# Kernel optimization log

Measured on AMD Instinct MI355X. Metric: run time of the kernel, lower is better.

## Reference

```python
import jax, jax.numpy as jnp
import numpy as np

B, C, H, W = 2, 48, 64, 64
EPS = 1e-5
ROW = [0, 0, 0, H // 4, H // 4, H // 4, H // 2, H // 2, H // 2]
COL = [0, W // 4, W // 2] * 3


def setup_inputs() -> dict:
    key = jax.random.key(0)
    ks = iter(jax.random.split(key, 40))
    s = 1.0 / np.sqrt(C)  # keep unscaled-softmax logits sane
    def rn(shape, scale=1.0):
        return jax.random.normal(next(ks), shape, jnp.float32) * scale
    def ru(shape):
        return jax.random.uniform(next(ks), shape, jnp.float32, 0.5, 1.5)
    return dict(
        input_feature=rn((B, C, H, W)), feat_b=rn((B, C, H, W)),
        feat_c=rn((B, C, H, W)), feat_d=rn((B, C, H, W)),
        W_fa_all=rn((C, C), s), W_fb_all=rn((C, C), s),
        W_fc_all=rn((C, C), s), W_fd_all=rn((C, C), s),
        W_fa=rn((9, C, C), s), W_fb=rn((9, C, C), s),
        W_fc=rn((9, C, C), s), W_fd=rn((9, C, C), s),
        fuse_w=rn((C, 4 * C), s), fuse_b=rn((C,), 0.1),
        fuse_g=ru((C,)), fuse_bb=rn((C,), 0.1), fuse_m=rn((C,), 0.1), fuse_v=ru((C,)),
        fuseP_w=rn((9, C, 4 * C), s), fuseP_b=rn((9, C), 0.1),
        fuseP_g=ru((9, C)), fuseP_bb=rn((9, C), 0.1), fuseP_m=rn((9, C), 0.1), fuseP_v=ru((9, C)),
        gamma_all=rn(()), gamma_p=rn((9,)),
        out_w=rn((C, C, 3, 3), s / 3.0), out_b=rn((C,), 0.1),
        out_g=ru((C,)), out_bb=rn((C,), 0.1), out_m=rn((C,), 0.1), out_v=ru((C,)),
    )


def _attn(q, k, v):
    # q,k,v: [..., C, N] -> energy [..., N, N]; non-standard softmax(max - energy)
    e = jnp.einsum('...cn,...cm->...nm', q, k)
    e = jnp.max(e, axis=-1, keepdims=True) - e
    a = jax.nn.softmax(e, axis=-1)
    return jnp.einsum('...cn,...nm->...cm', v, a)  # torch.matmul(v, attention)


def reference(input_feature, feat_b, feat_c, feat_d,
              W_fa_all, W_fb_all, W_fc_all, W_fd_all,
              W_fa, W_fb, W_fc, W_fd,
              fuse_w, fuse_b, fuse_g, fuse_bb, fuse_m, fuse_v,
              fuseP_w, fuseP_b, fuseP_g, fuseP_bb, fuseP_m, fuseP_v,
              gamma_all, gamma_p,
              out_w, out_b, out_g, out_bb, out_m, out_v):
    h2, w2 = H // 2, W // 2
    N = H * W
    # ---- global branch: channel-wise Linear (bias=False) applied over spatial tokens
    fa = jnp.einsum('dc,bcn->bdn', W_fa_all, input_feature.reshape(B, C, N))
    fb = jnp.einsum('dc,bcn->bdn', W_fb_all, feat_b.reshape(B, C, N))
    fc = jnp.einsum('dc,bcn->bdn', W_fc_all, feat_c.reshape(B, C, N))
    fd = jnp.einsum('dc,bcn->bdn', W_fd_all, feat_d.reshape(B, C, N))
    cat = jnp.concatenate([_attn(fa, fa, fa), _attn(fa, fb, fb),
                           _attn(fa, fc, fc), _attn(fa, fd, fd)], axis=1)
    cat = cat.reshape(B, 4 * C, H, W)
    y = jnp.einsum('oc,bchw->bohw', fuse_w, cat) + fuse_b[None, :, None, None]
    y = (y - fuse_m[:, None, None]) * (fuse_g / jnp.sqrt(fuse_v + EPS))[:, None, None] + fuse_bb[:, None, None]
    atten_all = jax.nn.relu(y)  # Dropout2d is identity at eval
    # ---- 9 overlapping patch branches, vectorized over the patch axis p
    def crops(x):
        return jnp.stack([x[:, :, r:r + h2, c:c + w2] for r, c in zip(ROW, COL)], 0).reshape(9, B, C, h2 * w2)
    pa = jnp.einsum('pdc,pbcn->pbdn', W_fa, crops(input_feature))
    pb = jnp.einsum('pdc,pbcn->pbdn', W_fb, crops(feat_b))
    pc = jnp.einsum('pdc,pbcn->pbdn', W_fc, crops(feat_c))
    pd = jnp.einsum('pdc,pbcn->pbdn', W_fd, crops(feat_d))
    pcat = jnp.concatenate([_attn(pa, pa, pa), _attn(pa, pb, pb),
                            _attn(pa, pc, pc), _attn(pa, pd, pd)], axis=2)
    pcat = pcat.reshape(9, B, 4 * C, h2, w2)
    py = jnp.einsum('poc,pbchw->pbohw', fuseP_w, pcat) + fuseP_b[:, None, :, None, None]
    py = ((py - fuseP_m[:, None, :, None, None])
          * (fuseP_g / jnp.sqrt(fuseP_v + EPS))[:, None, :, None, None]
          + fuseP_bb[:, None, :, None, None])
    patch_out = 0.5 * gamma_p[:, None, None, None, None] * jax.nn.relu(py)
    # ---- combine (overlapping patch regions accumulate additively, as in torch +=)
    out = input_feature + gamma_all * atten_all
    for i, (r, c) in enumerate(zip(ROW, COL)):
        out = out.at[:, :, r:r + h2, c:c + w2].add(patch_out[i])
    # ---- to_out: 3x3 conv + BN(eval) + ReLU
    z = jax.lax.conv_general_dilated(out, out_w, (1, 1), 'SAME',
                                     dimension_numbers=('NCHW', 'OIHW', 'NCHW'))
    z = z + out_b[None, :, None, None]
    z = (z - out_m[:, None, None]) * (out_g / jnp.sqrt(out_v + EPS))[:, None, None] + out_bb[:, None, None]
    return jax.nn.relu(z)
```

## Files before the change

kernel.cpp:

```cpp
#include <hip/hip_runtime.h>
#include <math.h>

typedef _Float16 f16;
typedef f16 f16x8 __attribute__((ext_vector_type(8)));
typedef float f32x4 __attribute__((ext_vector_type(4)));

namespace {
constexpr int B_ = 2, C_ = 48, H_ = 64, W_ = 64;
constexpr int N_ = H_ * W_;
constexpr int NP_ = 1024;
constexpr int C4_ = 4 * C_;
constexpr float EPS_ = 1e-5f;
constexpr float L2E_ = 1.44269504f;
constexpr float REFL2_ = -25.0f * 1.44269504f;
}

#define MFMA32(a, b, c) __builtin_amdgcn_mfma_f32_16x16x32_f16((a), (b), (c), 0, 0, 0)

__device__ inline float fast_exp2(float x) {
#if __has_builtin(__builtin_amdgcn_exp2f)
  return __builtin_amdgcn_exp2f(x);
#else
  float r;
  asm("v_exp_f32 %0, %1" : "=v"(r) : "v"(x));
  return r;
#endif
}

__global__ __launch_bounds__(256) void k_proj_g(
    const float* __restrict__ x0, const float* __restrict__ x1,
    const float* __restrict__ x2, const float* __restrict__ x3,
    const float* __restrict__ w0, const float* __restrict__ w1,
    const float* __restrict__ w2, const float* __restrict__ w3,
    f16* __restrict__ pn, f16* __restrict__ pt) {
  __shared__ float Ws[48 * 48];
  int tid = threadIdx.x;
  int b = blockIdx.y, X = blockIdx.z;
  const float* xp = X == 0 ? x0 : X == 1 ? x1 : X == 2 ? x2 : x3;
  const float* wp = X == 0 ? w0 : X == 1 ? w1 : X == 2 ? w2 : w3;
  for (int i = tid; i < 2304; i += 256) Ws[i] = wp[i];
  __syncthreads();
  int n = blockIdx.x * 256 + tid;
  const float* xb = xp + (size_t)b * 48 * 4096 + n;
  float acc[48];
#pragma unroll
  for (int d = 0; d < 48; ++d) acc[d] = 0.f;
  for (int c0 = 0; c0 < 48; c0 += 4) {
    float xv0 = xb[(size_t)(c0 + 0) * 4096];
    float xv1 = xb[(size_t)(c0 + 1) * 4096];
    float xv2 = xb[(size_t)(c0 + 2) * 4096];
    float xv3 = xb[(size_t)(c0 + 3) * 4096];
#pragma unroll
    for (int d = 0; d < 48; ++d) {
      const float4 wv = *(const float4*)&Ws[d * 48 + c0];
      acc[d] = fmaf(wv.x, xv0, fmaf(wv.y, xv1, fmaf(wv.z, xv2, fmaf(wv.w, xv3, acc[d]))));
    }
  }
  int z2 = X * 2 + b;
  f16* pnb = pn + ((size_t)z2 * 48) * 4096 + n;
#pragma unroll
  for (int d = 0; d < 48; ++d) pnb[(size_t)d * 4096] = (f16)acc[d];
  f16* ptb = pt + ((size_t)z2 * 4096 + n) * 64;
#pragma unroll
  for (int s = 0; s < 6; ++s) {
    f16x8 v;
#pragma unroll
    for (int j = 0; j < 8; ++j) v[j] = (f16)acc[s * 8 + j];
    *(f16x8*)(ptb + s * 8) = v;
  }
  f16x8 zv = {0, 0, 0, 0, 0, 0, 0, 0};
  *(f16x8*)(ptb + 48) = zv;
  *(f16x8*)(ptb + 56) = zv;
}

__global__ __launch_bounds__(256) void k_proj_p(
    const float* __restrict__ x0, const float* __restrict__ x1,
    const float* __restrict__ x2, const float* __restrict__ x3,
    const float* __restrict__ w0, const float* __restrict__ w1,
    const float* __restrict__ w2, const float* __restrict__ w3,
    f16* __restrict__ pn, f16* __restrict__ pt) {
  __shared__ float Ws[48 * 48];
  int tid = threadIdx.x;
  int p = blockIdx.y;
  int X = blockIdx.z >> 1, b = blockIdx.z & 1;
  const float* xp = X == 0 ? x0 : X == 1 ? x1 : X == 2 ? x2 : x3;
  const float* wp = (X == 0 ? w0 : X == 1 ? w1 : X == 2 ? w2 : w3) + (size_t)p * 2304;
  for (int i = tid; i < 2304; i += 256) Ws[i] = wp[i];
  __syncthreads();
  int t = blockIdx.x * 256 + tid;
  int r0 = (p / 3) * 16, c0w = (p % 3) * 16;
  int rr = r0 + (t >> 5), cc = c0w + (t & 31);
  const float* xb = xp + (size_t)b * 48 * 4096 + rr * 64 + cc;
  float acc[48];
#pragma unroll
  for (int d = 0; d < 48; ++d) acc[d] = 0.f;
  for (int c0 = 0; c0 < 48; c0 += 4) {
    float xv0 = xb[(size_t)(c0 + 0) * 4096];
    float xv1 = xb[(size_t)(c0 + 1) * 4096];
    float xv2 = xb[(size_t)(c0 + 2) * 4096];
    float xv3 = xb[(size_t)(c0 + 3) * 4096];
#pragma unroll
    for (int d = 0; d < 48; ++d) {
      const float4 wv = *(const float4*)&Ws[d * 48 + c0];
      acc[d] = fmaf(wv.x, xv0, fmaf(wv.y, xv1, fmaf(wv.z, xv2, fmaf(wv.w, xv3, acc[d]))));
    }
  }
  int z9 = (X * 2 + b) * 9 + p;
  f16* pnb = pn + ((size_t)z9 * 48) * 1024 + t;
#pragma unroll
  for (int d = 0; d < 48; ++d) pnb[(size_t)d * 1024] = (f16)acc[d];
  f16* ptb = pt + ((size_t)z9 * 1024 + t) * 64;
#pragma unroll
  for (int s = 0; s < 6; ++s) {
    f16x8 v;
#pragma unroll
    for (int j = 0; j < 8; ++j) v[j] = (f16)acc[s * 8 + j];
    *(f16x8*)(ptb + s * 8) = v;
  }
  f16x8 zv = {0, 0, 0, 0, 0, 0, 0, 0};
  *(f16x8*)(ptb + 48) = zv;
  *(f16x8*)(ptb + 56) = zv;
}

template <int NT, int NSPLIT, bool PATCH>
__global__ __launch_bounds__(256, 4) void k_stats_f(
    const f16* __restrict__ qT_all, const f16* __restrict__ kT_all,
    float* __restrict__ stp) {
  constexpr int MTI = (NT / NSPLIT) / 64;
  __shared__ uint4 Ks[2][512];
  int tid = threadIdx.x, wave = tid >> 6, lane = tid & 63, g = lane >> 4, lm = lane & 15;
  int by = blockIdx.y;
  int ms = by % NSPLIT, z = by / NSPLIT;
  const f16* qT;
  if (PATCH) {
    int b = (z / 9) % 2, p = z % 9;
    qT = qT_all + ((size_t)(b * 9 + p)) * NT * 64;
  } else {
    int b = z & 1;
    qT = qT_all + (size_t)b * NT * 64;
  }
  const f16* kT = kT_all + (size_t)z * NT * 64;
  int n0 = blockIdx.x * 128 + wave * 16;
  f16x8 aq0a = *(const f16x8*)(qT + (size_t)(n0 + lm) * 64 + g * 8);
  f16x8 aq1a = *(const f16x8*)(qT + (size_t)(n0 + lm) * 64 + 32 + g * 8);
  f16x8 aq0b = *(const f16x8*)(qT + (size_t)(n0 + 64 + lm) * 64 + g * 8);
  f16x8 aq1b = *(const f16x8*)(qT + (size_t)(n0 + 64 + lm) * 64 + 32 + g * 8);
  const int s0r = tid >> 3, s0c = (tid & 7) * 8;
  const int sw0 = tid ^ ((tid >> 3) & 7);
  const int sw1 = (tid + 256) ^ (((tid + 256) >> 3) & 7);
  const int swl = lm & 7;
  const int c0i = g ^ swl, c1i = (4 + g) ^ swl;
  int t_beg = ms * MTI;
  {
    const f16* src = kT + (size_t)t_beg * 64 * 64;
    Ks[0][sw0] = *(const uint4*)(src + (size_t)s0r * 64 + s0c);
    Ks[0][sw1] = *(const uint4*)(src + (size_t)(s0r + 32) * 64 + s0c);
  }
  __syncthreads();
  float zsa[4] = {0.f, 0.f, 0.f, 0.f};
  float zsb[4] = {0.f, 0.f, 0.f, 0.f};
  for (int mt = 0; mt < MTI; ++mt) {
    int cur = mt & 1;
    bool pf = (mt + 1 < MTI);
    uint4 k0v, k1v;
    if (pf) {
      const f16* src = kT + (size_t)(t_beg + mt + 1) * 64 * 64;
      k0v = *(const uint4*)(src + (size_t)s0r * 64 + s0c);
      k1v = *(const uint4*)(src + (size_t)(s0r + 32) * 64 + s0c);
    }
#pragma unroll
    for (int mf = 0; mf < 4; ++mf) {
      f16x8 b0 = __builtin_bit_cast(f16x8, Ks[cur][(16 * mf + lm) * 8 + c0i]);
      f16x8 b1 = __builtin_bit_cast(f16x8, Ks[cur][(16 * mf + lm) * 8 + c1i]);
      f32x4 ea = {0.f, 0.f, 0.f, 0.f};
      ea = MFMA32(aq0a, b0, ea);
      ea = MFMA32(aq1a, b1, ea);
      f32x4 eb = {0.f, 0.f, 0.f, 0.f};
      eb = MFMA32(aq0b, b0, eb);
      eb = MFMA32(aq1b, b1, eb);
#pragma unroll
      for (int r = 0; r < 4; ++r) {
        zsa[r] += fast_exp2(fmaf(ea[r], -L2E_, REFL2_));
        zsb[r] += fast_exp2(fmaf(eb[r], -L2E_, REFL2_));
      }
    }
    if (pf) {
      Ks[cur ^ 1][sw0] = k0v;
      Ks[cur ^ 1][sw1] = k1v;
    }
    __syncthreads();
  }
#pragma unroll
  for (int mask = 1; mask < 16; mask <<= 1) {
#pragma unroll
    for (int r = 0; r < 4; ++r) {
      zsa[r] += __shfl_xor(zsa[r], mask, 64);
      zsb[r] += __shfl_xor(zsb[r], mask, 64);
    }
  }
  if (lm == 0) {
#pragma unroll
    for (int r = 0; r < 4; ++r) {
      stp[((size_t)z * NT + n0 + 4 * g + r) * NSPLIT + ms] = zsa[r];
      stp[((size_t)z * NT + n0 + 64 + 4 * g + r) * NSPLIT + ms] = zsb[r];
    }
  }
}

template <int NSPLIT>
__global__ __launch_bounds__(256) void k_stats_merge(
    const float* __restrict__ stp, float* __restrict__ st, int rows) {
  int i = blockIdx.x * 256 + threadIdx.x;
  if (i >= rows) return;
  const float* p = stp + (size_t)i * NSPLIT;
  float Z = p[0];
#pragma unroll
  for (int j = 1; j < NSPLIT; ++j) Z += p[j];
  st[i] = REFL2_ - __log2f(Z);
}

template <int NT, int NSPLIT, bool PATCH>
__global__ __launch_bounds__(256, 4) void k_pv_f(
    const f16* __restrict__ qT_all, const f16* __restrict__ kT_all,
    const f16* __restrict__ vN_all, const float* __restrict__ st_all,
    float* __restrict__ out_all) {
  constexpr int CH = NT / NSPLIT;
  constexpr int NTI = CH / 64;
  __shared__ float As2[CH];
  __shared__ uint4 Qs[2][512];
  __shared__ uint4 Vs[2][384];
  __shared__ uint2 wt2[1024];
  int tid = threadIdx.x, wave = tid >> 6, lane = tid & 63, g = lane >> 4, lm = lane & 15;
  int by = blockIdx.y;
  int ns = by % NSPLIT, z = by / NSPLIT;
  const f16 *qT, *kT, *vN;
  float* op;
  if (PATCH) {
    int X = z / 18, b = (z / 9) % 2, p = z % 9;
    qT = qT_all + ((size_t)(b * 9 + p)) * NT * 64;
    op = out_all + ((size_t)((p * 2 + b) * C4_ + X * 48)) * NT;
  } else {
    int X = z >> 1, b = z & 1;
    qT = qT_all + (size_t)b * NT * 64;
    op = out_all + ((size_t)(b * C4_ + X * 48)) * NT;
  }
  kT = kT_all + (size_t)z * NT * 64;
  vN = vN_all + (size_t)z * 48 * NT;
  const float* st = st_all + (size_t)z * NT + ns * CH;
  ((float4*)As2)[tid] = ((const float4*)st)[tid];
  int mwa = blockIdx.x * 128 + wave * 16;
  int mwb = mwa + 64;
  f16x8 bk0a = *(const f16x8*)(kT + (size_t)(mwa + lm) * 64 + g * 8);
  f16x8 bk1a = *(const f16x8*)(kT + (size_t)(mwa + lm) * 64 + 32 + g * 8);
  f16x8 bk0b = *(const f16x8*)(kT + (size_t)(mwb + lm) * 64 + g * 8);
  f16x8 bk1b = *(const f16x8*)(kT + (size_t)(mwb + lm) * 64 + 32 + g * 8);
  const int s0r = tid >> 3, s0c = (tid & 7) * 8;
  const int sw0 = tid ^ ((tid >> 3) & 7);
  const int sw1 = (tid + 256) ^ (((tid + 256) >> 3) & 7);
  const int swl = lm & 7;
  const int c0i = g ^ swl, c1i = (4 + g) ^ swl;
  int t_beg = ns * NTI;
  {
    const f16* qsrc = qT + (size_t)t_beg * 64 * 64;
    Qs[0][sw0] = *(const uint4*)(qsrc + (size_t)s0r * 64 + s0c);
    Qs[0][sw1] = *(const uint4*)(qsrc + (size_t)(s0r + 32) * 64 + s0c);
    Vs[0][sw0] = *(const uint4*)(vN + (size_t)s0r * NT + t_beg * 64 + s0c);
    if (tid < 128)
      Vs[0][sw1] = *(const uint4*)(vN + (size_t)(s0r + 32) * NT + t_beg * 64 + s0c);
  }
  __syncthreads();
  f32x4 oa0 = {0.f, 0.f, 0.f, 0.f}, oa1 = {0.f, 0.f, 0.f, 0.f}, oa2 = {0.f, 0.f, 0.f, 0.f};
  f32x4 ob0 = {0.f, 0.f, 0.f, 0.f}, ob1 = {0.f, 0.f, 0.f, 0.f}, ob2 = {0.f, 0.f, 0.f, 0.f};
  int wbuf = wave * 256;
  int rb = wbuf + lm * 16;
  for (int nt = 0; nt < NTI; ++nt) {
    int cur = nt & 1;
    bool pf = (nt + 1 < NTI);
    uint4 q0v, q1v, v0v, v1v;
    if (pf) {
      int tn = t_beg + nt + 1;
      const f16* qsrc = qT + (size_t)tn * 64 * 64;
      q0v = *(const uint4*)(qsrc + (size_t)s0r * 64 + s0c);
      q1v = *(const uint4*)(qsrc + (size_t)(s0r + 32) * 64 + s0c);
      v0v = *(const uint4*)(vN + (size_t)s0r * NT + tn * 64 + s0c);
      if (tid < 128)
        v1v = *(const uint4*)(vN + (size_t)(s0r + 32) * NT + tn * 64 + s0c);
    }
    f16x8 av0[3], av1[3];
#pragma unroll
    for (int cf = 0; cf < 3; ++cf) {
      av0[cf] = __builtin_bit_cast(f16x8, Vs[cur][(16 * cf + lm) * 8 + c0i]);
      av1[cf] = __builtin_bit_cast(f16x8, Vs[cur][(16 * cf + lm) * 8 + c1i]);
    }
    {
      f32x4 e[4];
#pragma unroll
      for (int nf = 0; nf < 4; ++nf) {
        f16x8 a0 = __builtin_bit_cast(f16x8, Qs[cur][(16 * nf + lm) * 8 + c0i]);
        f16x8 a1 = __builtin_bit_cast(f16x8, Qs[cur][(16 * nf + lm) * 8 + c1i]);
        f32x4 t = {0.f, 0.f, 0.f, 0.f};
        t = MFMA32(a0, bk0a, t);
        t = MFMA32(a1, bk1a, t);
        e[nf] = t;
      }
#pragma unroll
      for (int nf = 0; nf < 4; ++nf) {
        float4 a4 = *(const float4*)&As2[nt * 64 + nf * 16 + g * 4];
        float w0 = fast_exp2(fmaf(e[nf][0], -L2E_, a4.x));
        float w1 = fast_exp2(fmaf(e[nf][1], -L2E_, a4.y));
        float w2 = fast_exp2(fmaf(e[nf][2], -L2E_, a4.z));
        float w3 = fast_exp2(fmaf(e[nf][3], -L2E_, a4.w));
        unsigned lo = __builtin_bit_cast(unsigned, __builtin_amdgcn_cvt_pkrtz(w0, w1));
        unsigned hi = __builtin_bit_cast(unsigned, __builtin_amdgcn_cvt_pkrtz(w2, w3));
        int s = 2 * nf + (g >> 1);
        wt2[wbuf + lm * 16 + ((s ^ swl) * 2) + (g & 1)] = make_uint2(lo, hi);
      }
      __builtin_amdgcn_sched_barrier(0);
      f16x8 bw0 = __builtin_bit_cast(f16x8, *(const uint4*)&wt2[rb + c0i * 2]);
      f16x8 bw1 = __builtin_bit_cast(f16x8, *(const uint4*)&wt2[rb + c1i * 2]);
      oa0 = MFMA32(av0[0], bw0, oa0); oa0 = MFMA32(av1[0], bw1, oa0);
      oa1 = MFMA32(av0[1], bw0, oa1); oa1 = MFMA32(av1[1], bw1, oa1);
      oa2 = MFMA32(av0[2], bw0, oa2); oa2 = MFMA32(av1[2], bw1, oa2);
    }
    __builtin_amdgcn_sched_barrier(0);
    {
      f32x4 e[4];
#pragma unroll
      for (int nf = 0; nf < 4; ++nf) {
        f16x8 a0 = __builtin_bit_cast(f16x8, Qs[cur][(16 * nf + lm) * 8 + c0i]);
        f16x8 a1 = __builtin_bit_cast(f16x8, Qs[cur][(16 * nf + lm) * 8 + c1i]);
        f32x4 t = {0.f, 0.f, 0.f, 0.f};
        t = MFMA32(a0, bk0b, t);
        t = MFMA32(a1, bk1b, t);
        e[nf] = t;
      }
#pragma unroll
      for (int nf = 0; nf < 4; ++nf) {
        float4 a4 = *(const float4*)&As2[nt * 64 + nf * 16 + g * 4];
        float w0 = fast_exp2(fmaf(e[nf][0], -L2E_, a4.x));
        float w1 = fast_exp2(fmaf(e[nf][1], -L2E_, a4.y));
        float w2 = fast_exp2(fmaf(e[nf][2], -L2E_, a4.z));
        float w3 = fast_exp2(fmaf(e[nf][3], -L2E_, a4.w));
        unsigned lo = __builtin_bit_cast(unsigned, __builtin_amdgcn_cvt_pkrtz(w0, w1));
        unsigned hi = __builtin_bit_cast(unsigned, __builtin_amdgcn_cvt_pkrtz(w2, w3));
        int s = 2 * nf + (g >> 1);
        wt2[wbuf + lm * 16 + ((s ^ swl) * 2) + (g & 1)] = make_uint2(lo, hi);
      }
      __builtin_amdgcn_sched_barrier(0);
      f16x8 bw0 = __builtin_bit_cast(f16x8, *(const uint4*)&wt2[rb + c0i * 2]);
      f16x8 bw1 = __builtin_bit_cast(f16x8, *(const uint4*)&wt2[rb + c1i * 2]);
      ob0 = MFMA32(av0[0], bw0, ob0); ob0 = MFMA32(av1[0], bw1, ob0);
      ob1 = MFMA32(av0[1], bw0, ob1); ob1 = MFMA32(av1[1], bw1, ob1);
      ob2 = MFMA32(av0[2], bw0, ob2); ob2 = MFMA32(av1[2], bw1, ob2);
    }
    if (pf) {
      Qs[cur ^ 1][sw0] = q0v;
      Qs[cur ^ 1][sw1] = q1v;
      Vs[cur ^ 1][sw0] = v0v;
      if (tid < 128) Vs[cur ^ 1][sw1] = v1v;
    }
    __syncthreads();
  }
  if (NSPLIT == 1) {
#pragma unroll
    for (int r = 0; r < 4; ++r) {
      op[(size_t)(0 + 4 * g + r) * NT + mwa + lm] = oa0[r];
      op[(size_t)(16 + 4 * g + r) * NT + mwa + lm] = oa1[r];
      op[(size_t)(32 + 4 * g + r) * NT + mwa + lm] = oa2[r];
      op[(size_t)(0 + 4 * g + r) * NT + mwb + lm] = ob0[r];
      op[(size_t)(16 + 4 * g + r) * NT + mwb + lm] = ob1[r];
      op[(size_t)(32 + 4 * g + r) * NT + mwb + lm] = ob2[r];
    }
  } else {
#pragma unroll
    for (int r = 0; r < 4; ++r) {
      atomicAdd(&op[(size_t)(0 + 4 * g + r) * NT + mwa + lm], oa0[r]);
      atomicAdd(&op[(size_t)(16 + 4 * g + r) * NT + mwa + lm], oa1[r]);
      atomicAdd(&op[(size_t)(32 + 4 * g + r) * NT + mwa + lm], oa2[r]);
      atomicAdd(&op[(size_t)(0 + 4 * g + r) * NT + mwb + lm], ob0[r]);
      atomicAdd(&op[(size_t)(16 + 4 * g + r) * NT + mwb + lm], ob1[r]);
      atomicAdd(&op[(size_t)(32 + 4 * g + r) * NT + mwb + lm], ob2[r]);
    }
  }
}

__global__ __launch_bounds__(256) void k_fuse_global(
    const float* __restrict__ cat, const float* __restrict__ fw,
    const float* __restrict__ fb, const float* __restrict__ fg,
    const float* __restrict__ fbb, const float* __restrict__ fm,
    const float* __restrict__ fv, const float* __restrict__ gamma_all,
    const float* __restrict__ input, float* __restrict__ comb) {
  int idx = blockIdx.x * 256 + threadIdx.x;
  int n4 = idx & 1023;
  int rest = idx >> 10;
  int o = rest % C_;
  int b = rest / C_;
  const float* cr = cat + (size_t)b * C4_ * N_ + n4 * 4;
  const float* wr = fw + (size_t)o * C4_;
  float4 acc = {0.f, 0.f, 0.f, 0.f};
#pragma unroll 8
  for (int c = 0; c < C4_; ++c) {
    float4 xv = *(const float4*)(cr + (size_t)c * N_);
    float w = wr[c];
    acc.x = fmaf(w, xv.x, acc.x); acc.y = fmaf(w, xv.y, acc.y);
    acc.z = fmaf(w, xv.z, acc.z); acc.w = fmaf(w, xv.w, acc.w);
  }
  float scale = fg[o] * rsqrtf(fv[o] + EPS_);
  float sh = fb[o] - fm[o], bb = fbb[o], ga = gamma_all[0];
  float4 inv = *(const float4*)(input + ((size_t)(b * C_ + o) * N_) + n4 * 4);
  float4 out;
  out.x = inv.x + ga * fmaxf((acc.x + sh) * scale + bb, 0.f);
  out.y = inv.y + ga * fmaxf((acc.y + sh) * scale + bb, 0.f);
  out.z = inv.z + ga * fmaxf((acc.z + sh) * scale + bb, 0.f);
  out.w = inv.w + ga * fmaxf((acc.w + sh) * scale + bb, 0.f);
  *(float4*)(comb + ((size_t)(b * C_ + o) * N_) + n4 * 4) = out;
}

__global__ __launch_bounds__(256) void k_fuse_patch(
    const float* __restrict__ pcat, const float* __restrict__ fw,
    const float* __restrict__ fb, const float* __restrict__ fg,
    const float* __restrict__ fbb, const float* __restrict__ fm,
    const float* __restrict__ fv, const float* __restrict__ gamma_p,
    float* __restrict__ py) {
  int idx = blockIdx.x * 256 + threadIdx.x;
  int t4 = idx & 255;
  int rest = idx >> 8;
  int o = rest % C_; rest /= C_;
  int b = rest % B_;
  int p = rest / B_;
  const float* cr = pcat + ((size_t)(p * B_ + b) * C4_) * NP_ + t4 * 4;
  const float* wr = fw + (size_t)(p * C_ + o) * C4_;
  float4 acc = {0.f, 0.f, 0.f, 0.f};
#pragma unroll 8
  for (int c = 0; c < C4_; ++c) {
    float4 xv = *(const float4*)(cr + (size_t)c * NP_);
    float w = wr[c];
    acc.x = fmaf(w, xv.x, acc.x); acc.y = fmaf(w, xv.y, acc.y);
    acc.z = fmaf(w, xv.z, acc.z); acc.w = fmaf(w, xv.w, acc.w);
  }
  int po = p * C_ + o;
  float scale = fg[po] * rsqrtf(fv[po] + EPS_);
  float sh = fb[po] - fm[po], bb = fbb[po], gp = 0.5f * gamma_p[p];
  float4 out;
  out.x = gp * fmaxf((acc.x + sh) * scale + bb, 0.f);
  out.y = gp * fmaxf((acc.y + sh) * scale + bb, 0.f);
  out.z = gp * fmaxf((acc.z + sh) * scale + bb, 0.f);
  out.w = gp * fmaxf((acc.w + sh) * scale + bb, 0.f);
  *(float4*)(py + ((size_t)(p * B_ + b) * C_ + o) * NP_ + t4 * 4) = out;
}

__global__ __launch_bounds__(256) void k_combine(
    const float* __restrict__ py, const float* __restrict__ comb,
    f16* __restrict__ combh) {
  int idx = blockIdx.x * 256 + threadIdx.x;
  int w = idx & (W_ - 1);
  int h = (idx >> 6) & (H_ - 1);
  int rest = idx >> 12;
  int ch = rest % C_;
  int b = rest / C_;
  float val = comb[idx];
#pragma unroll
  for (int p = 0; p < 9; ++p) {
    int r0 = (p / 3) * 16, c0 = (p % 3) * 16;
    if (h >= r0 && h < r0 + 32 && w >= c0 && w < c0 + 32)
      val += py[((size_t)(p * B_ + b) * C_ + ch) * NP_ + (h - r0) * 32 + (w - c0)];
  }
  combh[idx] = (f16)val;
}

__global__ __launch_bounds__(256) void k_conv2(
    const f16* __restrict__ combh, const float* __restrict__ cw,
    const float* __restrict__ cb, const float* __restrict__ cg,
    const float* __restrict__ cbb, const float* __restrict__ cm,
    const float* __restrict__ cv, float* __restrict__ out) {
  __shared__ uint4 inh[2304];
  int tid = threadIdx.x;
  int h0 = blockIdx.x * 4, ocg = blockIdx.y, b = blockIdx.z;
  for (int i = tid; i < 2304; i += 256) {
    int c = i / 48;
    int rem = i - c * 48;
    int r = rem >> 3, u = rem & 7;
    int hh = h0 - 1 + r;
    uint4 val = make_uint4(0, 0, 0, 0);
    if (hh >= 0 && hh < H_)
      val = *(const uint4*)(combh + (((size_t)(b * C_ + c) * H_ + hh) * W_ + u * 8));
    inh[i] = val;
  }
  __syncthreads();
  int w = tid & 63, dh = tid >> 6;
  float acc[6] = {0.f, 0.f, 0.f, 0.f, 0.f, 0.f};
  const f16* lds = (const f16*)inh;
  int wm = w > 0 ? w - 1 : 0;
  int wp = w < 63 ? w + 1 : 63;
  for (int c = 0; c < 48; ++c) {
    float v[9];
#pragma unroll
    for (int r = 0; r < 3; ++r) {
      const f16* row = lds + (size_t)(c * 6 + dh + r) * 64;
      float lf = (float)row[wm];
      float md = (float)row[w];
      float rt = (float)row[wp];
      v[r * 3 + 0] = (w > 0) ? lf : 0.f;
      v[r * 3 + 1] = md;
      v[r * 3 + 2] = (w < 63) ? rt : 0.f;
    }
#pragma unroll
    for (int j = 0; j < 6; ++j) {
      const float* wr = cw + (size_t)((ocg * 6 + j) * 48 + c) * 9;
#pragma unroll
      for (int k = 0; k < 9; ++k) acc[j] = fmaf(v[k], wr[k], acc[j]);
    }
  }
#pragma unroll
  for (int j = 0; j < 6; ++j) {
    int o = ocg * 6 + j;
    float scale = cg[o] * rsqrtf(cv[o] + EPS_);
    float y = (acc[j] + cb[o] - cm[o]) * scale + cbb[o];
    out[(size_t)(b * C_ + o) * N_ + (h0 + dh) * 64 + w] = fmaxf(y, 0.f);
  }
}

extern "C" void kernel_launch(void* const* d_in, const int* in_sizes, int n_in,
                              void* d_out, int out_size, void* d_ws, size_t ws_size,
                              hipStream_t stream) {
  (void)in_sizes; (void)n_in; (void)out_size; (void)ws_size;
  const float* x[4];
  const float* Wall[4];
  const float* Wp[4];
  for (int i = 0; i < 4; ++i) {
    x[i] = (const float*)d_in[i];
    Wall[i] = (const float*)d_in[4 + i];
    Wp[i] = (const float*)d_in[8 + i];
  }
  const float* fuse_w = (const float*)d_in[12];
  const float* fuse_b = (const float*)d_in[13];
  const float* fuse_g = (const float*)d_in[14];
  const float* fuse_bb = (const float*)d_in[15];
  const float* fuse_m = (const float*)d_in[16];
  const float* fuse_v = (const float*)d_in[17];
  const float* fuseP_w = (const float*)d_in[18];
  const float* fuseP_b = (const float*)d_in[19];
  const float* fuseP_g = (const float*)d_in[20];
  const float* fuseP_bb = (const float*)d_in[21];
  const float* fuseP_m = (const float*)d_in[22];
  const float* fuseP_v = (const float*)d_in[23];
  const float* gamma_all = (const float*)d_in[24];
  const float* gamma_p = (const float*)d_in[25];
  const float* out_w = (const float*)d_in[26];
  const float* out_b = (const float*)d_in[27];
  const float* out_g = (const float*)d_in[28];
  const float* out_bb = (const float*)d_in[29];
  const float* out_m = (const float*)d_in[30];
  const float* out_v = (const float*)d_in[31];

  char* base = (char*)d_ws;
  size_t off = 0;
  auto carve = [&](size_t bytes) {
    char* p = base + off;
    off += (bytes + 255) & ~(size_t)255;
    return p;
  };
  f16* projg_n = (f16*)carve((size_t)8 * 48 * N_ * 2);
  f16* projg_t = (f16*)carve((size_t)8 * N_ * 64 * 2);
  f16* projp_n = (f16*)carve((size_t)72 * 48 * NP_ * 2);
  f16* projp_t = (f16*)carve((size_t)72 * NP_ * 64 * 2);
  float* stpg = (float*)carve((size_t)8 * N_ * 4 * 4);
  float* stpp = (float*)carve((size_t)72 * NP_ * 4);
  float* statsg = (float*)carve((size_t)8 * N_ * 4);
  float* statsp = (float*)carve((size_t)72 * NP_ * 4);
  float* cat = (float*)carve((size_t)B_ * C4_ * N_ * 4);
  float* pcat = (float*)carve((size_t)9 * B_ * C4_ * NP_ * 4);
  float* comb = (float*)carve((size_t)B_ * C_ * N_ * 4);
  float* py = (float*)carve((size_t)9 * B_ * C_ * NP_ * 4);
  f16* combh = (f16*)carve((size_t)B_ * C_ * N_ * 2);

  dim3 blk(256);

  k_proj_g<<<dim3(16, 2, 4), blk, 0, stream>>>(
      x[0], x[1], x[2], x[3], Wall[0], Wall[1], Wall[2], Wall[3], projg_n, projg_t);
  k_proj_p<<<dim3(4, 9, 8), blk, 0, stream>>>(
      x[0], x[1], x[2], x[3], Wp[0], Wp[1], Wp[2], Wp[3], projp_n, projp_t);

  k_stats_f<N_, 4, false><<<dim3(32, 32), blk, 0, stream>>>(projg_t, projg_t, stpg);
  k_stats_f<NP_, 1, true><<<dim3(8, 72), blk, 0, stream>>>(projp_t, projp_t, stpp);
  k_stats_merge<4><<<dim3((8 * N_) / 256), blk, 0, stream>>>(stpg, statsg, 8 * N_);
  k_stats_merge<1><<<dim3((72 * NP_) / 256), blk, 0, stream>>>(stpp, statsp, 72 * NP_);

  (void)hipMemsetAsync(cat, 0, (size_t)B_ * C4_ * N_ * sizeof(float), stream);
  k_pv_f<N_, 4, false><<<dim3(32, 32), blk, 0, stream>>>(
      projg_t, projg_t, projg_n, statsg, cat);
  k_pv_f<NP_, 1, true><<<dim3(8, 72), blk, 0, stream>>>(
      projp_t, projp_t, projp_n, statsp, pcat);

  k_fuse_global<<<(B_ * C_ * (N_ / 4)) / 256, blk, 0, stream>>>(
      cat, fuse_w, fuse_b, fuse_g, fuse_bb, fuse_m, fuse_v, gamma_all, x[0], comb);
  k_fuse_patch<<<(9 * B_ * C_ * (NP_ / 4)) / 256, blk, 0, stream>>>(
      pcat, fuseP_w, fuseP_b, fuseP_g, fuseP_bb, fuseP_m, fuseP_v, gamma_p, py);
  k_combine<<<(B_ * C_ * N_) / 256, blk, 0, stream>>>(py, comb, combh);
  k_conv2<<<dim3(16, 8, 2), blk, 0, stream>>>(
      combh, out_w, out_b, out_g, out_bb, out_m, out_v, (float*)d_out);
}
```

Baseline: 285.9 us.

## Single-buffer Q/V tiles, merge both half-tiles per step, split patch attention in two

The PV kernel drops the double-buffered Q/V shared tiles in favour of single buffers with an extra barrier, and handles both 64-column halves in one pass: it computes both energy tiles, writes both weight tiles to a doubled per-wave buffer, then runs the PV MFMAs together. The patch branch's stats and PV kernels are split along the key dimension (NSPLIT=2), doubling the grid. This needs an extra memset of pcat and atomic accumulation. The aim is more parallelism for the small patch problem and more independent MFMA work per iteration, at the cost of losing load/compute overlap from double buffering and adding atomics.

Measured after the change: 294.0 us. 1.03x slower.

```diff
diff --git a/kernel.cpp b/kernel.cpp
--- a/kernel.cpp
+++ b/kernel.cpp
@@ -227,9 +227,9 @@
   constexpr int CH = NT / NSPLIT;
   constexpr int NTI = CH / 64;
   __shared__ float As2[CH];
-  __shared__ uint4 Qs[2][512];
-  __shared__ uint4 Vs[2][384];
-  __shared__ uint2 wt2[1024];
+  __shared__ uint4 Qs[512];
+  __shared__ uint4 Vs[384];
+  __shared__ uint2 wt2[2048];
   int tid = threadIdx.x, wave = tid >> 6, lane = tid & 63, g = lane >> 4, lm = lane & 15;
   int by = blockIdx.y;
   int ns = by % NSPLIT, z = by / NSPLIT;
@@ -247,7 +247,7 @@
   kT = kT_all + (size_t)z * NT * 64;
   vN = vN_all + (size_t)z * 48 * NT;
   const float* st = st_all + (size_t)z * NT + ns * CH;
-  ((float4*)As2)[tid] = ((const float4*)st)[tid];
+  if (tid < CH / 4) ((float4*)As2)[tid] = ((const float4*)st)[tid];
   int mwa = blockIdx.x * 128 + wave * 16;
   int mwb = mwa + 64;
   f16x8 bk0a = *(const f16x8*)(kT + (size_t)(mwa + lm) * 64 + g * 8);
@@ -262,19 +262,20 @@
   int t_beg = ns * NTI;
   {
     const f16* qsrc = qT + (size_t)t_beg * 64 * 64;
-    Qs[0][sw0] = *(const uint4*)(qsrc + (size_t)s0r * 64 + s0c);
-    Qs[0][sw1] = *(const uint4*)(qsrc + (size_t)(s0r + 32) * 64 + s0c);
-    Vs[0][sw0] = *(const uint4*)(vN + (size_t)s0r * NT + t_beg * 64 + s0c);
+    Qs[sw0] = *(const uint4*)(qsrc + (size_t)s0r * 64 + s0c);
+    Qs[sw1] = *(const uint4*)(qsrc + (size_t)(s0r + 32) * 64 + s0c);
+    Vs[sw0] = *(const uint4*)(vN + (size_t)s0r * NT + t_beg * 64 + s0c);
     if (tid < 128)
-      Vs[0][sw1] = *(const uint4*)(vN + (size_t)(s0r + 32) * NT + t_beg * 64 + s0c);
+      Vs[sw1] = *(const uint4*)(vN + (size_t)(s0r + 32) * NT + t_beg * 64 + s0c);
   }
   __syncthreads();
   f32x4 oa0 = {0.f, 0.f, 0.f, 0.f}, oa1 = {0.f, 0.f, 0.f, 0.f}, oa2 = {0.f, 0.f, 0.f, 0.f};
   f32x4 ob0 = {0.f, 0.f, 0.f, 0.f}, ob1 = {0.f, 0.f, 0.f, 0.f}, ob2 = {0.f, 0.f, 0.f, 0.f};
-  int wbuf = wave * 256;
-  int rb = wbuf + lm * 16;
+  int wbufa = wave * 512;
+  int wbufb = wave * 512 + 256;
+  int rba = wbufa + lm * 16;
+  int rbb = wbufb + lm * 16;
   for (int nt = 0; nt < NTI; ++nt) {
-    int cur = nt & 1;
     bool pf = (nt + 1 < NTI);
     uint4 q0v, q1v, v0v, v1v;
     if (pf) {
@@ -286,78 +287,68 @@
       if (tid < 128)
         v1v = *(const uint4*)(vN + (size_t)(s0r + 32) * NT + tn * 64 + s0c);
     }
-    f16x8 av0[3], av1[3];
+    f32x4 ea[4], eb[4];
+#pragma unroll
+    for (int nf = 0; nf < 4; ++nf) {
+      f16x8 a0 = __builtin_bit_cast(f16x8, Qs[(16 * nf + lm) * 8 + c0i]);
+      f16x8 a1 = __builtin_bit_cast(f16x8, Qs[(16 * nf + lm) * 8 + c1i]);
+      f32x4 ta = {0.f, 0.f, 0.f, 0.f};
+      ta = MFMA32(a0, bk0a, ta);
+      ta = MFMA32(a1, bk1a, ta);
+      ea[nf] = ta;
+      f32x4 tb = {0.f, 0.f, 0.f, 0.f};
+      tb = MFMA32(a0, bk0b, tb);
+      tb = MFMA32(a1, bk1b, tb);
+      eb[nf] = tb;
+    }
+#pragma unroll
+    for (int nf = 0; nf < 4; ++nf) {
+      float4 a4 = *(const float4*)&As2[nt * 64 + nf * 16 + g * 4];
+      float wa0 = fast_exp2(fmaf(ea[nf][0], -L2E_, a4.x));
+      float wa1 = fast_exp2(fmaf(ea[nf][1], -L2E_, a4.y));
+      float wa2 = fast_exp2(fmaf(ea[nf][2], -L2E_, a4.z));
+      float wa3 = fast_exp2(fmaf(ea[nf][3], -L2E_, a4.w));
+      float wb0 = fast_exp2(fmaf(eb[nf][0], -L2E_, a4.x));
+      float wb1 = fast_exp2(fmaf(eb[nf][1], -L2E_, a4.y));
+      float wb2 = fast_exp2(fmaf(eb[nf][2], -L2E_, a4.z));
+      float wb3 = fast_exp2(fmaf(eb[nf][3], -L2E_, a4.w));
+      unsigned la = __builtin_bit_cast(unsigned, __builtin_amdgcn_cvt_pkrtz(wa0, wa1));
+      unsigned ha = __builtin_bit_cast(unsigned, __builtin_amdgcn_cvt_pkrtz(wa2, wa3));
+      unsigned lb = __builtin_bit_cast(unsigned, __builtin_amdgcn_cvt_pkrtz(wb0, wb1));
+      unsigned hb = __builtin_bit_cast(unsigned, __builtin_amdgcn_cvt_pkrtz(wb2, wb3));
+      int s = 2 * nf + (g >> 1);
+      int so = ((s ^ swl) * 2) + (g & 1);
+      wt2[wbufa + lm * 16 + so] = make_uint2(la, ha);
+      wt2[wbufb + lm * 16 + so] = make_uint2(lb, hb);
+    }
+    __builtin_amdgcn_sched_barrier(0);
+    f16x8 bw0a = __builtin_bit_cast(f16x8, *(const uint4*)&wt2[rba + c0i * 2]);
+    f16x8 bw1a = __builtin_bit_cast(f16x8, *(const uint4*)&wt2[rba + c1i * 2]);
+    f16x8 bw0b = __builtin_bit_cast(f16x8, *(const uint4*)&wt2[rbb + c0i * 2]);
+    f16x8 bw1b = __builtin_bit_cast(f16x8, *(const uint4*)&wt2[rbb + c1i * 2]);
 #pragma unroll
     for (int cf = 0; cf < 3; ++cf) {
-      av0[cf] = __builtin_bit_cast(f16x8, Vs[cur][(16 * cf + lm) * 8 + c0i]);
-      av1[cf] = __builtin_bit_cast(f16x8, Vs[cur][(16 * cf + lm) * 8 + c1i]);
-    }
-    {
-      f32x4 e[4];
-#pragma unroll
-      for (int nf = 0; nf < 4; ++nf) {
-        f16x8 a0 = __builtin_bit_cast(f16x8, Qs[cur][(16 * nf + lm) * 8 + c0i]);
-        f16x8 a1 = __builtin_bit_cast(f16x8, Qs[cur][(16 * nf + lm) * 8 + c1i]);
-        f32x4 t = {0.f, 0.f, 0.f, 0.f};
-        t = MFMA32(a0, bk0a, t);
-        t = MFMA32(a1, bk1a, t);
-        e[nf] = t;
+      f16x8 av0 = __builtin_bit_cast(f16x8, Vs[(16 * cf + lm) * 8 + c0i]);
+      f16x8 av1 = __builtin_bit_cast(f16x8, Vs[(16 * cf + lm) * 8 + c1i]);
+      if (cf == 0) {
+        oa0 = MFMA32(av0, bw0a, oa0); oa0 = MFMA32(av1, bw1a, oa0);
+        ob0 = MFMA32(av0, bw0b, ob0); ob0 = MFMA32(av1, bw1b, ob0);
       }
-#pragma unroll
-      for (int nf = 0; nf < 4; ++nf) {
-        float4 a4 = *(const float4*)&As2[nt * 64 + nf * 16 + g * 4];
-        float w0 = fast_exp2(fmaf(e[nf][0], -L2E_, a4.x));
-        float w1 = fast_exp2(fmaf(e[nf][1], -L2E_, a4.y));
-        float w2 = fast_exp2(fmaf(e[nf][2], -L2E_, a4.z));
-        float w3 = fast_exp2(fmaf(e[nf][3], -L2E_, a4.w));
-        unsigned lo = __builtin_bit_cast(unsigned, __builtin_amdgcn_cvt_pkrtz(w0, w1));
-        unsigned hi = __builtin_bit_cast(unsigned, __builtin_amdgcn_cvt_pkrtz(w2, w3));
-        int s = 2 * nf + (g >> 1);
-        wt2[wbuf + lm * 16 + ((s ^ swl) * 2) + (g & 1)] = make_uint2(lo, hi);
+      if (cf == 1) {
+        oa1 = MFMA32(av0, bw0a, oa1); oa1 = MFMA32(av1, bw1a, oa1);
+        ob1 = MFMA32(av0, bw0b, ob1); ob1 = MFMA32(av1, bw1b, ob1);
       }
-      __builtin_amdgcn_sched_barrier(0);
-      f16x8 bw0 = __builtin_bit_cast(f16x8, *(const uint4*)&wt2[rb + c0i * 2]);
-      f16x8 bw1 = __builtin_bit_cast(f16x8, *(const uint4*)&wt2[rb + c1i * 2]);
-      oa0 = MFMA32(av0[0], bw0, oa0); oa0 = MFMA32(av1[0], bw1, oa0);
-      oa1 = MFMA32(av0[1], bw0, oa1); oa1 = MFMA32(av1[1], bw1, oa1);
-      oa2 = MFMA32(av0[2], bw0, oa2); oa2 = MFMA32(av1[2], bw1, oa2);
-    }
-    __builtin_amdgcn_sched_barrier(0);
-    {
-      f32x4 e[4];
-#pragma unroll
-      for (int nf = 0; nf < 4; ++nf) {
-        f16x8 a0 = __builtin_bit_cast(f16x8, Qs[cur][(16 * nf + lm) * 8 + c0i]);
-        f16x8 a1 = __builtin_bit_cast(f16x8, Qs[cur][(16 * nf + lm) * 8 + c1i]);
-        f32x4 t = {0.f, 0.f, 0.f, 0.f};
-        t = MFMA32(a0, bk0b, t);
-        t = MFMA32(a1, bk1b, t);
-        e[nf] = t;
+      if (cf == 2) {
+        oa2 = MFMA32(av0, bw0a, oa2); oa2 = MFMA32(av1, bw1a, oa2);
+        ob2 = MFMA32(av0, bw0b, ob2); ob2 = MFMA32(av1, bw1b, ob2);
       }
-#pragma unroll
-      for (int nf = 0; nf < 4; ++nf) {
-        float4 a4 = *(const float4*)&As2[nt * 64 + nf * 16 + g * 4];
-        float w0 = fast_exp2(fmaf(e[nf][0], -L2E_, a4.x));
-        float w1 = fast_exp2(fmaf(e[nf][1], -L2E_, a4.y));
-        float w2 = fast_exp2(fmaf(e[nf][2], -L2E_, a4.z));
-        float w3 = fast_exp2(fmaf(e[nf][3], -L2E_, a4.w));
-        unsigned lo = __builtin_bit_cast(unsigned, __builtin_amdgcn_cvt_pkrtz(w0, w1));
-        unsigned hi = __builtin_bit_cast(unsigned, __builtin_amdgcn_cvt_pkrtz(w2, w3));
-        int s = 2 * nf + (g >> 1);
-        wt2[wbuf + lm * 16 + ((s ^ swl) * 2) + (g & 1)] = make_uint2(lo, hi);
-      }
-      __builtin_amdgcn_sched_barrier(0);
-      f16x8 bw0 = __builtin_bit_cast(f16x8, *(const uint4*)&wt2[rb + c0i * 2]);
-      f16x8 bw1 = __builtin_bit_cast(f16x8, *(const uint4*)&wt2[rb + c1i * 2]);
-      ob0 = MFMA32(av0[0], bw0, ob0); ob0 = MFMA32(av1[0], bw1, ob0);
-      ob1 = MFMA32(av0[1], bw0, ob1); ob1 = MFMA32(av1[1], bw1, ob1);
-      ob2 = MFMA32(av0[2], bw0, ob2); ob2 = MFMA32(av1[2], bw1, ob2);
-    }
+    }
+    __syncthreads();
     if (pf) {
-      Qs[cur ^ 1][sw0] = q0v;
-      Qs[cur ^ 1][sw1] = q1v;
-      Vs[cur ^ 1][sw0] = v0v;
-      if (tid < 128) Vs[cur ^ 1][sw1] = v1v;
+      Qs[sw0] = q0v;
+      Qs[sw1] = q1v;
+      Vs[sw0] = v0v;
+      if (tid < 128) Vs[sw1] = v1v;
     }
     __syncthreads();
   }
@@ -565,7 +556,7 @@
   f16* projp_n = (f16*)carve((size_t)72 * 48 * NP_ * 2);
   f16* projp_t = (f16*)carve((size_t)72 * NP_ * 64 * 2);
   float* stpg = (float*)carve((size_t)8 * N_ * 4 * 4);
-  float* stpp = (float*)carve((size_t)72 * NP_ * 4);
+  float* stpp = (float*)carve((size_t)72 * NP_ * 2 * 4);
   float* statsg = (float*)carve((size_t)8 * N_ * 4);
   float* statsp = (float*)carve((size_t)72 * NP_ * 4);
   float* cat = (float*)carve((size_t)B_ * C4_ * N_ * 4);
@@ -582,14 +573,15 @@
       x[0], x[1], x[2], x[3], Wp[0], Wp[1], Wp[2], Wp[3], projp_n, projp_t);
 
   k_stats_f<N_, 4, false><<<dim3(32, 32), blk, 0, stream>>>(projg_t, projg_t, stpg);
-  k_stats_f<NP_, 1, true><<<dim3(8, 72), blk, 0, stream>>>(projp_t, projp_t, stpp);
+  k_stats_f<NP_, 2, true><<<dim3(8, 144), blk, 0, stream>>>(projp_t, projp_t, stpp);
   k_stats_merge<4><<<dim3((8 * N_) / 256), blk, 0, stream>>>(stpg, statsg, 8 * N_);
-  k_stats_merge<1><<<dim3((72 * NP_) / 256), blk, 0, stream>>>(stpp, statsp, 72 * NP_);
+  k_stats_merge<2><<<dim3((72 * NP_) / 256), blk, 0, stream>>>(stpp, statsp, 72 * NP_);
 
   (void)hipMemsetAsync(cat, 0, (size_t)B_ * C4_ * N_ * sizeof(float), stream);
+  (void)hipMemsetAsync(pcat, 0, (size_t)9 * B_ * C4_ * NP_ * sizeof(float), stream);
   k_pv_f<N_, 4, false><<<dim3(32, 32), blk, 0, stream>>>(
       projg_t, projg_t, projg_n, statsg, cat);
-  k_pv_f<NP_, 1, true><<<dim3(8, 72), blk, 0, stream>>>(
+  k_pv_f<NP_, 2, true><<<dim3(8, 144), blk, 0, stream>>>(
       projp_t, projp_t, projp_n, statsp, pcat);
 
   k_fuse_global<<<(B_ * C_ * (N_ / 4)) / 256, blk, 0, stream>>>(
```
